# Optimization experiments

Hardware: AMD Instinct MI355X
Metric: run time of the kernel (lower is better)

The kernel has to match this reference:

```python
import jax, jax.numpy as jnp
import numpy as np

BN_EPS = 1e-5

def setup_inputs() -> dict:
    key = jax.random.key(0)
    k0, k1, k2, k3, k4 = jax.random.split(key, 5)
    B, N, D, E = 8, 256, 128, 4096
    x_l = jax.random.normal(k0, (B, N, D), dtype=jnp.float32)
    src = jax.random.randint(k1, (E,), 0, N)
    dst = jax.random.randint(k2, (E,), 0, N)
    edge_index_l = jnp.stack([src, dst], axis=0)  # [2, E]
    mask_l = jax.random.randint(k3, (B, N), 0, 2).astype(bool)
    W = jax.random.normal(k4, (D, D), dtype=jnp.float32) * (1.0 / np.sqrt(D))
    b = jnp.zeros((D,), jnp.float32)
    gamma = jnp.ones((D,), jnp.float32)
    beta = jnp.zeros((D,), jnp.float32)
    return {"x_l": x_l, "edge_index_l": edge_index_l, "mask_l": mask_l,
            "W": W, "b": b, "gamma": gamma, "beta": beta}


def reference(x_l, edge_index_l, mask_l, W, b, gamma, beta):
    # x_l: [B, N, D]; edge_index_l: [2, E]; mask_l: [B, N] bool
    B, N, D = x_l.shape
    src, dst = edge_index_l[0], edge_index_l[1]
    # Vectorized replacement of the Python edge loop: edges with dst - src == 3
    # zero the mask at both endpoints (the explicit interaction zeroing in the
    # original is subsumed by the mask, since masked entries never survive).
    cov = (dst - src) == 3  # [E] bool
    hit = jnp.zeros((N,), bool)
    hit = hit.at[src].max(cov)
    hit = hit.at[dst].max(cov)
    mask = mask_l & ~hit[None, :]  # [B, N]
    # Pairwise mask: outer AND minus diagonal
    eye = jnp.eye(N, dtype=bool)
    pair_mask = (mask[:, :, None] & mask[:, None, :]) & ~eye[None]  # [B, N, N]
    # Outer-product interaction: [B, N, N, D]
    interaction = x_l[:, :, None, :] * x_l[:, None, :, :]
    # Linear
    h = jnp.einsum('bijd,ed->bije', interaction, W) + b
    # BatchNorm1d over the masked (selected) rows, training-mode batch stats.
    m = pair_mask[..., None].astype(h.dtype)  # [B, N, N, 1]
    cnt = jnp.maximum(jnp.sum(m), 1.0)
    mean = jnp.sum(h * m, axis=(0, 1, 2)) / cnt  # [D]
    var = jnp.sum(m * (h - mean) ** 2, axis=(0, 1, 2)) / cnt  # biased, as torch BN
    hn = (h - mean) * jax.lax.rsqrt(var + BN_EPS) * gamma + beta
    # Dropout is identity in eval mode; LeakyReLU slope 0.01 (torch default).
    out = jax.nn.leaky_relu(hn, negative_slope=0.01) * m  # zero non-selected entries
    return out, pair_mask
```

## Files before the change

### kernel.cpp

```cpp
#include <hip/hip_runtime.h>

#define B_ 8
#define N_ 256
#define D_ 128
#define E_ 4096

typedef __attribute__((ext_vector_type(8))) short bf16x8;
typedef __attribute__((ext_vector_type(4))) float f32x4;
typedef __attribute__((ext_vector_type(2))) float f32x2;

__device__ inline unsigned int pack2bf(float lo, float hi) {
    unsigned ul = __float_as_uint(lo);
    ul = ul + 0x7FFFu + ((ul >> 16) & 1u);
    unsigned uh = __float_as_uint(hi);
    uh = uh + 0x7FFFu + ((uh >> 16) & 1u);
    return (ul >> 16) | (uh & 0xFFFF0000u);
}

__device__ inline unsigned short f2bf(float f) {
    unsigned u = __float_as_uint(f);
    u = u + 0x7FFFu + ((u >> 16) & 1u);
    return (unsigned short)(u >> 16);
}


__global__ __launch_bounds__(256) void k_prep(const void* __restrict__ edges_raw,
                                              const void* __restrict__ mask_raw,
                                              const float* __restrict__ W,
                                              int* __restrict__ mask,
                                              int* __restrict__ jlist,
                                              int* __restrict__ jcnt,
                                              unsigned short* __restrict__ Wb,
                                              float* __restrict__ Wt,
                                              float* __restrict__ tq,
                                              float* __restrict__ dq) {
    int blk = blockIdx.x, tid = threadIdx.x;
    if (blk >= B_) {
        int idx = (blk - B_) * 256 + tid;
        if (idx < 16384) {
            float w = W[idx];
            Wb[idx] = f2bf(w);
            int e = idx >> 7, d = idx & 127;
            Wt[d * D_ + e] = w;
        } else if (idx < 16512) tq[idx - 16384] = 0.0f;
        else dq[idx - 16512] = 0.0f;
        return;
    }
    int b = blk;
    __shared__ unsigned char hit[N_];
    __shared__ int flags[2];
    __shared__ int wcnt[4], wbase[4];
    hit[tid] = 0;
    if (tid < 2) flags[tid] = 0;
    __syncthreads();

    const unsigned char* mb = (const unsigned char*)mask_raw;
    int loc_m = 0;
    for (int idx = tid; idx < B_ * N_; idx += 256)
        if ((idx & 3) && mb[idx]) loc_m = 1;
    if (loc_m) flags[0] = 1;
    const int* e32 = (const int*)edges_raw;
    int loc_e = 0;
    for (int idx = tid; idx < 2 * E_; idx += 256)
        if ((idx & 1) && e32[idx]) loc_e = 1;
    if (loc_e) flags[1] = 1;
    __syncthreads();

    int mask_is_u8 = flags[0], e_is_i32 = flags[1];
    const long long* e64 = (const long long*)edges_raw;
    for (int e = tid; e < E_; e += 256) {
        int s, d;
        if (e_is_i32) { s = e32[e]; d = e32[E_ + e]; }
        else          { s = (int)e64[e]; d = (int)e64[E_ + e]; }
        if (d - s == 3) { hit[s] = 1; hit[d] = 1; }
    }
    __syncthreads();

    const int* m32 = (const int*)mask_raw;
    int lane = tid & 63, wid = tid >> 6;
    int raw = mask_is_u8 ? (int)(mb[b * N_ + tid] != 0) : (int)(m32[b * N_ + tid] != 0);
    int m = raw && (hit[tid] == 0);
    mask[b * N_ + tid] = m;
    unsigned long long bal = __ballot(m);
    if (lane == 0) wcnt[wid] = __popcll(bal);
    __syncthreads();
    if (tid == 0) {
        int base = 0;
        for (int w = 0; w < 4; ++w) { wbase[w] = base; base += wcnt[w]; }
        jcnt[b] = base;
    }
    __syncthreads();
    if (m) {
        int pos = wbase[wid] + __popcll(bal & ((1ull << lane) - 1ull));
        jlist[b * N_ + pos] = tid;
    }
}

__global__ __launch_bounds__(128) void k_gram3(const float* __restrict__ x,
                                               const int* __restrict__ jlist,
                                               const int* __restrict__ jcnt,
                                               float* __restrict__ part,
                                               float* __restrict__ s1,
                                               float* __restrict__ cdiag) {
    int d = blockIdx.x, b = blockIdx.y, dp = threadIdx.x;
    int kc = jcnt[b];
    const int* jl = jlist + b * N_;
    const float* xb = x + (size_t)b * N_ * D_;
    float c0 = 0, c1 = 0, q0 = 0, q1 = 0, s0 = 0, s1a = 0;
    int t = 0;
    for (; t + 1 < kc; t += 2) {
        int i0 = jl[t], i1 = jl[t + 1];
        float xd0 = xb[i0 * D_ + d], xp0 = xb[i0 * D_ + dp];
        float xd1 = xb[i1 * D_ + d], xp1 = xb[i1 * D_ + dp];
        c0 += xd0 * xp0; q0 += (xd0 * xd0) * (xp0 * xp0); s0 += xd0;
        c1 += xd1 * xp1; q1 += (xd1 * xd1) * (xp1 * xp1); s1a += xd1;
    }
    if (t < kc) {
        int i0 = jl[t];
        float xd0 = xb[i0 * D_ + d], xp0 = xb[i0 * D_ + dp];
        c0 += xd0 * xp0; q0 += (xd0 * xd0) * (xp0 * xp0); s0 += xd0;
    }
    float c = c0 + c1, q = q0 + q1, sa = s0 + s1a;
    part[((size_t)b * D_ + d) * D_ + dp] = c * c - q;
    if (dp == d) cdiag[b * D_ + d] = c;
    if (dp == 0) s1[b * D_ + d] = sa;
}

__global__ __launch_bounds__(128) void k_mw2(const float* __restrict__ part,
                                             const float* __restrict__ Wt,
                                             const float* __restrict__ s1,
                                             const float* __restrict__ cdiag,
                                             float* __restrict__ tq,
                                             float* __restrict__ dq) {
    __shared__ float Ms[D_];
    __shared__ float svs;
    int d = blockIdx.x, e = threadIdx.x;
    float m = 0.0f;
#pragma unroll
    for (int b = 0; b < B_; ++b) m += part[((size_t)b * D_ + d) * D_ + e];
    Ms[e] = m;
    if (e == 0) {
        float sv = 0.0f;
#pragma unroll
        for (int b = 0; b < B_; ++b) {
            float s = s1[b * D_ + d];
            sv += s * s - cdiag[b * D_ + d];
        }
        svs = sv;
    }
    __syncthreads();
    float y = 0.0f;
#pragma unroll 8
    for (int p = 0; p < D_; ++p) y += Ms[p] * Wt[p * D_ + e];
    float wed = Wt[d * D_ + e];
    atomicAdd(tq + e, wed * y);
    atomicAdd(dq + e, wed * svs);
}

__global__ __launch_bounds__(256) void k_main(const float* __restrict__ x,
                                              const int* __restrict__ mask,
                                              const int* __restrict__ jlist,
                                              const int* __restrict__ jcnt,
                                              const unsigned short* __restrict__ Wb,
                                              const float* __restrict__ tq,
                                              const float* __restrict__ dq,
                                              const float* __restrict__ bvec,
                                              const float* __restrict__ gamma,
                                              const float* __restrict__ beta,
                                              float* __restrict__ out,
                                              float* __restrict__ pair) {
    __shared__ int msk[N_];
    __shared__ int jls[N_];
    __shared__ float scs[D_], shs[D_];

    int b = blockIdx.y, i = blockIdx.x;
    int tid = threadIdx.x;
    int mi = mask[b * N_ + i];

    f32x4 z4 = (f32x4)(0.f);
    f32x4* outrow = (f32x4*)(out + (size_t)(b * N_ + i) * N_ * D_);

    if (!mi) {
        __builtin_nontemporal_store(0.0f, &pair[(size_t)(b * N_ + i) * N_ + tid]);
#pragma unroll
        for (int p = 0; p < 32; ++p)
            __builtin_nontemporal_store(z4, &outrow[tid + 256 * p]);
        return;
    }

    msk[tid] = mask[b * N_ + tid];
    jls[tid] = jlist[b * N_ + tid];

    if (tid < D_) {
        float cnt = 0.0f;
#pragma unroll
        for (int bb = 0; bb < B_; ++bb) {
            float k = (float)jcnt[bb];
            cnt += k * k - k;
        }
        if (cnt < 1.0f) cnt = 1.0f;
        float be = bvec[tid];
        float mean = dq[tid] / cnt + be;
        float eh2 = tq[tid] / cnt + 2.0f * be * mean - be * be;
        float var = eh2 - mean * mean;
        if (var < 0.0f) var = 0.0f;
        float s = gamma[tid] * rsqrtf(var + 1e-5f);
        scs[tid] = s;
        shs[tid] = be * s + beta[tid] - mean * s;
    }
    __syncthreads();

    float pm = (msk[tid] && tid != i) ? 1.0f : 0.0f;
    __builtin_nontemporal_store(pm, &pair[(size_t)(b * N_ + i) * N_ + tid]);

    {
        int c = tid & 31, g = tid >> 5;
        for (int j = g; j < N_; j += 8)
            if (!msk[j] || j == i)
                __builtin_nontemporal_store(z4, &outrow[j * 32 + c]);
    }

    int w = tid >> 6, l = tid & 63;
    int lo16 = l & 15, hi4 = l >> 4;
    int E0 = w * 32;

    const float* xi = x + (size_t)(b * N_ + i) * D_;

    float4 xi0[4], xi1[4];
#pragma unroll
    for (int ks = 0; ks < 4; ++ks) {
        int d = ks * 32 + hi4 * 8;
        xi0[ks] = *(const float4*)(xi + d);
        xi1[ks] = *(const float4*)(xi + d + 4);
    }

    bf16x8 bfrag[2][4];
#pragma unroll
    for (int et = 0; et < 2; ++et) {
        int e = E0 + 2 * lo16 + et;
#pragma unroll
        for (int ks = 0; ks < 4; ++ks)
            bfrag[et][ks] = *(const bf16x8*)(Wb + (size_t)e * D_ + ks * 32 + hi4 * 8);
    }

    float sc0 = scs[E0 + 2 * lo16], sh0 = shs[E0 + 2 * lo16];
    float sc1 = scs[E0 + 2 * lo16 + 1], sh1 = shs[E0 + 2 * lo16 + 1];

    int kc = jcnt[b];
    const float* xb = x + (size_t)b * N_ * D_;
    float* outbase = out + (size_t)(b * N_ + i) * N_ * D_;

    for (int jt = 0; jt < kc; jt += 64) {
#pragma unroll
        for (int jq = 0; jq < 4; ++jq) {
            int idx = jt + jq * 16 + lo16;
            int cidx = idx < kc ? idx : kc - 1;
            const float* xj = xb + (size_t)jls[cidx] * D_;

            f32x4 acc0 = (f32x4)(0.f);
            f32x4 acc1 = (f32x4)(0.f);
#pragma unroll
            for (int ks = 0; ks < 4; ++ks) {
                int d = ks * 32 + hi4 * 8;
                float4 a0 = *(const float4*)(xj + d);
                float4 a1 = *(const float4*)(xj + d + 4);
                uint4 pk;
                pk.x = pack2bf(a0.x * xi0[ks].x, a0.y * xi0[ks].y);
                pk.y = pack2bf(a0.z * xi0[ks].z, a0.w * xi0[ks].w);
                pk.z = pack2bf(a1.x * xi1[ks].x, a1.y * xi1[ks].y);
                pk.w = pack2bf(a1.z * xi1[ks].z, a1.w * xi1[ks].w);
                bf16x8 afr = *(bf16x8*)&pk;
                acc0 = __builtin_amdgcn_mfma_f32_16x16x32_bf16(afr, bfrag[0][ks], acc0, 0, 0, 0);
                acc1 = __builtin_amdgcn_mfma_f32_16x16x32_bf16(afr, bfrag[1][ks], acc1, 0, 0, 0);
            }

#pragma unroll
            for (int v = 0; v < 4; ++v) {
                int jrow = jt + jq * 16 + hi4 * 4 + v;
                if (jrow < kc) {
                    int j = jls[jrow];
                    if (j != i) {
                        float h0 = acc0[v] * sc0 + sh0;
                        float h1 = acc1[v] * sc1 + sh1;
                        f32x2 o;
                        o.x = h0 >= 0.f ? h0 : 0.01f * h0;
                        o.y = h1 >= 0.f ? h1 : 0.01f * h1;
                        __builtin_nontemporal_store(o,
                            (f32x2*)(outbase + (size_t)j * D_ + E0 + 2 * lo16));
                    }
                }
            }
        }
    }
}

extern "C" void kernel_launch(void* const* d_in, const int* in_sizes, int n_in,
                              void* d_out, int out_size, void* d_ws, size_t ws_size,
                              hipStream_t stream) {
    const float* x = (const float*)d_in[0];
    const void* edges = d_in[1];
    const void* mask_in = d_in[2];
    const float* W = (const float*)d_in[3];
    const float* bvec = (const float*)d_in[4];
    const float* gamma = (const float*)d_in[5];
    const float* beta = (const float*)d_in[6];

    float* out = (float*)d_out;
    float* pair = out + (size_t)B_ * N_ * N_ * D_;

    char* ws = (char*)d_ws;
    int* mask = (int*)(ws + 0);
    int* jlist = (int*)(ws + 8192);
    int* jcnt = (int*)(ws + 16384);
    float* tq = (float*)(ws + 16448);
    float* dq = (float*)(ws + 16960);
    unsigned short* Wb = (unsigned short*)(ws + 17472);
    float* Wt = (float*)(ws + 50240);
    float* s1 = (float*)(ws + 115776);
    float* cdiag = (float*)(ws + 119872);
    float* part = (float*)(ws + 123968);

    k_prep<<<73, 256, 0, stream>>>(edges, mask_in, W, mask, jlist, jcnt, Wb, Wt, tq, dq);
    {
        dim3 g(D_, B_);
        k_gram3<<<g, 128, 0, stream>>>(x, jlist, jcnt, part, s1, cdiag);
    }
    k_mw2<<<128, 128, 0, stream>>>(part, Wt, s1, cdiag, tq, dq);
    {
        dim3 g(N_, B_);
        k_main<<<g, 256, 0, stream>>>(x, mask, jlist, jcnt, Wb, tq, dq,
                                      bvec, gamma, beta, out, pair);
    }
}
```

Baseline: 113.2 us.

## Split zero-fill into separate interleaved blocks and stage products in LDS

The main kernel now launches a 1D grid where one in every five blocks does the compute for a row (b,i) and the other four write the zero entries of the output, each covering a 64-wide j chunk. Zeroing work is spread across more blocks instead of serialized inside compute blocks. The elementwise products x_i*x_j are computed once per 32-row tile, packed to bf16 and stored in a swizzled LDS buffer, where the MFMA A fragments are read. Before, every lane recomputed them from global loads. This adds two barriers per tile and more blocks, but should cut redundant global loads and balance the store-heavy work.

New measurement: 94.84 us. 16.2% less time.

```diff
diff --git a/kernel.cpp b/kernel.cpp
--- a/kernel.cpp
+++ b/kernel.cpp
@@ -157,7 +157,7 @@
     atomicAdd(dq + e, wed * svs);
 }
 
-__global__ __launch_bounds__(256) void k_main(const float* __restrict__ x,
+__global__ __launch_bounds__(256) void k_mega(const float* __restrict__ x,
                                               const int* __restrict__ mask,
                                               const int* __restrict__ jlist,
                                               const int* __restrict__ jcnt,
@@ -171,20 +171,38 @@
                                               float* __restrict__ pair) {
     __shared__ int msk[N_];
     __shared__ int jls[N_];
+    __shared__ __align__(16) unsigned char Vsb[32 * 256];
     __shared__ float scs[D_], shs[D_];
 
-    int b = blockIdx.y, i = blockIdx.x;
-    int tid = threadIdx.x;
+    int blk = blockIdx.x, tid = threadIdx.x;
+    int q5 = blk / 5;
+    f32x4 z4 = (f32x4)(0.f);
+
+    if (blk != q5 * 5) {
+        int zblk = blk - q5 - 1;
+        int r0 = zblk * 64;
+        int j0 = r0 & 255;
+        int i = (r0 >> 8) & 255;
+        int b = r0 >> 16;
+        int mi = mask[b * N_ + i];
+        f32x4* outrow = (f32x4*)(out + (size_t)(b * N_ + i) * N_ * D_);
+        int c = tid & 31, g = tid >> 5;
+#pragma unroll
+        for (int p = 0; p < 8; ++p) {
+            int j = j0 + g + 8 * p;
+            int mj = mask[b * N_ + j];
+            if (!mi || !mj || j == i)
+                __builtin_nontemporal_store(z4, &outrow[(size_t)j * 32 + c]);
+        }
+        return;
+    }
+
+    int cblk = q5;
+    int b = cblk >> 8, i = cblk & 255;
     int mi = mask[b * N_ + i];
-
-    f32x4 z4 = (f32x4)(0.f);
-    f32x4* outrow = (f32x4*)(out + (size_t)(b * N_ + i) * N_ * D_);
 
     if (!mi) {
         __builtin_nontemporal_store(0.0f, &pair[(size_t)(b * N_ + i) * N_ + tid]);
-#pragma unroll
-        for (int p = 0; p < 32; ++p)
-            __builtin_nontemporal_store(z4, &outrow[tid + 256 * p]);
         return;
     }
 
@@ -213,27 +231,10 @@
     float pm = (msk[tid] && tid != i) ? 1.0f : 0.0f;
     __builtin_nontemporal_store(pm, &pair[(size_t)(b * N_ + i) * N_ + tid]);
 
-    {
-        int c = tid & 31, g = tid >> 5;
-        for (int j = g; j < N_; j += 8)
-            if (!msk[j] || j == i)
-                __builtin_nontemporal_store(z4, &outrow[j * 32 + c]);
-    }
-
     int w = tid >> 6, l = tid & 63;
     int lo16 = l & 15, hi4 = l >> 4;
     int E0 = w * 32;
 
-    const float* xi = x + (size_t)(b * N_ + i) * D_;
-
-    float4 xi0[4], xi1[4];
-#pragma unroll
-    for (int ks = 0; ks < 4; ++ks) {
-        int d = ks * 32 + hi4 * 8;
-        xi0[ks] = *(const float4*)(xi + d);
-        xi1[ks] = *(const float4*)(xi + d + 4);
-    }
-
     bf16x8 bfrag[2][4];
 #pragma unroll
     for (int et = 0; et < 2; ++et) {
@@ -247,33 +248,57 @@
     float sc1 = scs[E0 + 2 * lo16 + 1], sh1 = shs[E0 + 2 * lo16 + 1];
 
     int kc = jcnt[b];
+    const float* xi = x + (size_t)(b * N_ + i) * D_;
     const float* xb = x + (size_t)b * N_ * D_;
     float* outbase = out + (size_t)(b * N_ + i) * N_ * D_;
 
-    for (int jt = 0; jt < kc; jt += 64) {
-#pragma unroll
-        for (int jq = 0; jq < 4; ++jq) {
-            int idx = jt + jq * 16 + lo16;
-            int cidx = idx < kc ? idx : kc - 1;
-            const float* xj = xb + (size_t)jls[cidx] * D_;
-
+    for (int jt = 0; jt < kc; jt += 32) {
+        __syncthreads();
+        int jn = kc - jt; if (jn > 32) jn = 32;
+
+        {
+            int r = tid >> 3, q = tid & 7;
+            int jrow = jt + r;
+            bool ok = (r < jn);
+            const float* xj = ok ? (xb + (size_t)jls[jrow] * D_) : xi;
+            int d0 = q * 16;
+            int rx = (r & 7) << 4;
+            float4 a0 = *(const float4*)(xj + d0);
+            float4 a1 = *(const float4*)(xj + d0 + 4);
+            float4 a2 = *(const float4*)(xj + d0 + 8);
+            float4 a3 = *(const float4*)(xj + d0 + 12);
+            float4 b0 = *(const float4*)(xi + d0);
+            float4 b1 = *(const float4*)(xi + d0 + 4);
+            float4 b2 = *(const float4*)(xi + d0 + 8);
+            float4 b3 = *(const float4*)(xi + d0 + 12);
+            uint4 pk1, pk2;
+            pk1.x = pack2bf(a0.x * b0.x, a0.y * b0.y);
+            pk1.y = pack2bf(a0.z * b0.z, a0.w * b0.w);
+            pk1.z = pack2bf(a1.x * b1.x, a1.y * b1.y);
+            pk1.w = pack2bf(a1.z * b1.z, a1.w * b1.w);
+            pk2.x = pack2bf(a2.x * b2.x, a2.y * b2.y);
+            pk2.y = pack2bf(a2.z * b2.z, a2.w * b2.w);
+            pk2.z = pack2bf(a3.x * b3.x, a3.y * b3.y);
+            pk2.w = pack2bf(a3.z * b3.z, a3.w * b3.w);
+            if (!ok) { pk1 = make_uint4(0, 0, 0, 0); pk2 = pk1; }
+            *(uint4*)(Vsb + r * 256 + ((2 * d0) ^ rx)) = pk1;
+            *(uint4*)(Vsb + r * 256 + ((2 * (d0 + 8)) ^ rx)) = pk2;
+        }
+        __syncthreads();
+
+#pragma unroll
+        for (int jq = 0; jq < 2; ++jq) {
             f32x4 acc0 = (f32x4)(0.f);
             f32x4 acc1 = (f32x4)(0.f);
+            int rA = jq * 16 + lo16;
+            int rbase = rA * 256;
+            int rx = (rA & 7) << 4;
 #pragma unroll
             for (int ks = 0; ks < 4; ++ks) {
-                int d = ks * 32 + hi4 * 8;
-                float4 a0 = *(const float4*)(xj + d);
-                float4 a1 = *(const float4*)(xj + d + 4);
-                uint4 pk;
-                pk.x = pack2bf(a0.x * xi0[ks].x, a0.y * xi0[ks].y);
-                pk.y = pack2bf(a0.z * xi0[ks].z, a0.w * xi0[ks].w);
-                pk.z = pack2bf(a1.x * xi1[ks].x, a1.y * xi1[ks].y);
-                pk.w = pack2bf(a1.z * xi1[ks].z, a1.w * xi1[ks].w);
-                bf16x8 afr = *(bf16x8*)&pk;
+                bf16x8 afr = *(const bf16x8*)(Vsb + rbase + ((ks * 64 + hi4 * 16) ^ rx));
                 acc0 = __builtin_amdgcn_mfma_f32_16x16x32_bf16(afr, bfrag[0][ks], acc0, 0, 0, 0);
                 acc1 = __builtin_amdgcn_mfma_f32_16x16x32_bf16(afr, bfrag[1][ks], acc1, 0, 0, 0);
             }
-
 #pragma unroll
             for (int v = 0; v < 4; ++v) {
                 int jrow = jt + jq * 16 + hi4 * 4 + v;
@@ -326,9 +351,6 @@
         k_gram3<<<g, 128, 0, stream>>>(x, jlist, jcnt, part, s1, cdiag);
     }
     k_mw2<<<128, 128, 0, stream>>>(part, Wt, s1, cdiag, tq, dq);
-    {
-        dim3 g(N_, B_);
-        k_main<<<g, 256, 0, stream>>>(x, mask, jlist, jcnt, Wb, tq, dq,
+    k_mega<<<10240, 256, 0, stream>>>(x, mask, jlist, jcnt, Wb, tq, dq,
                                       bvec, gamma, beta, out, pair);
-    }
-}
+}
```
